# Performance work log

Measured on AMD Instinct MI355X. Metric: run time of the kernel, lower is better.

The kernel has to match this reference:

```python
import jax, jax.numpy as jnp
import numpy as np
import math

H = 64   # hidden_size
N = 512  # num_objects
B = 128  # batch


def setup_inputs() -> dict:
    key = jax.random.key(0)
    ks = jax.random.split(key, 10)
    q = jax.random.normal(ks[0], (N, B, H), dtype=jnp.float32)
    k = jax.random.normal(ks[1], (N, B, H), dtype=jnp.float32)
    v = jax.random.normal(ks[2], (N, B, H), dtype=jnp.float32)
    # binary visibility mask [B, N, N]
    batch_traffic_id_map = (jax.random.uniform(ks[3], (B, N, N)) < 0.7).astype(jnp.float32)
    s = 1.0 / math.sqrt(H)
    Wq = jax.random.uniform(ks[4], (H, H), minval=-s, maxval=s, dtype=jnp.float32)
    bq = jax.random.uniform(ks[5], (H,), minval=-s, maxval=s, dtype=jnp.float32)
    Wk = jax.random.uniform(ks[6], (H, H), minval=-s, maxval=s, dtype=jnp.float32)
    bk = jax.random.uniform(ks[7], (H,), minval=-s, maxval=s, dtype=jnp.float32)
    Wv = jax.random.uniform(ks[8], (H, H), minval=-s, maxval=s, dtype=jnp.float32)
    bv = jax.random.uniform(ks[9], (H,), minval=-s, maxval=s, dtype=jnp.float32)
    return {"q": q, "k": k, "v": v, "batch_traffic_id_map": batch_traffic_id_map,
            "Wq": Wq, "bq": bq, "Wk": Wk, "bk": bk, "Wv": Wv, "bv": bv}


def reference(q, k, v, batch_traffic_id_map, Wq, bq, Wk, bk, Wv, bv):
    hidden_size = q.shape[-1]
    # Linear projections then transpose(0,1): [N,B,H] -> [B,N,H]
    qp = jnp.einsum('nbh,kh->bnk', q, Wq) + bq
    kp = jnp.einsum('nbh,kh->bnk', k, Wk) + bk
    vp = jnp.einsum('nbh,kh->bnk', v, Wv) + bv
    # scaled scores, exp, mask, custom sum-normalization
    a = jnp.einsum('bnh,bmh->bnm', qp, kp) / jnp.sqrt(jnp.float32(hidden_size))
    a = jnp.exp(a) * batch_traffic_id_map
    a_sum = jnp.sum(a, axis=-1)                      # [B, N]
    a_sum = jnp.where(a_sum == 0, jnp.ones_like(a_sum), a_sum)
    A = a / a_sum[..., None]                          # [B, N, N]
    out = jnp.einsum('bnm,bmh->nbh', A, vp)           # matmul + transpose(0,1)
    # dropout is identity in eval mode
    return out, A
```

## Files before the change

kernel.cpp:

```cpp
#include <hip/hip_runtime.h>

#define H 64
#define NOBJ 512
#define BATCH 128

typedef __attribute__((ext_vector_type(8))) short s16x8;
typedef __attribute__((ext_vector_type(4))) float f32x4;
typedef __attribute__((ext_vector_type(4))) unsigned short u16x4;
typedef __attribute__((ext_vector_type(8))) unsigned short u16x8;

__device__ __forceinline__ unsigned short f2bf(float f) {
    unsigned int u = __float_as_uint(f);
    u += 0x7FFFu + ((u >> 16) & 1u);
    return (unsigned short)(u >> 16);
}
__device__ __forceinline__ float bf2f(unsigned short h) {
    return __uint_as_float((unsigned int)h << 16);
}

#define MFMA16(a, b, c) __builtin_amdgcn_mfma_f32_16x16x32_bf16(a, b, c, 0, 0, 0)

__global__ __launch_bounds__(256) void mask_pack_kernel(
    const float* __restrict__ mask, unsigned int* __restrict__ bits)
{
    __shared__ unsigned char nib[256];
    const int tid = threadIdx.x;
    const size_t base = (size_t)blockIdx.x * 1024;
    const float4 f = *(const float4*)(mask + base + (size_t)tid * 4);
    nib[tid] = (unsigned char)((unsigned)(f.x != 0.0f)
             | ((unsigned)(f.y != 0.0f) << 1)
             | ((unsigned)(f.z != 0.0f) << 2)
             | ((unsigned)(f.w != 0.0f) << 3));
    __syncthreads();
    if (tid < 32) {
        unsigned int wv = 0;
        #pragma unroll
        for (int i = 0; i < 8; ++i)
            wv |= (unsigned int)nib[tid * 8 + i] << (4 * i);
        bits[base / 32 + tid] = wv;
    }
}

__global__ __launch_bounds__(256) void proj_kernel(
    const float* __restrict__ q, const float* __restrict__ k, const float* __restrict__ v,
    const float* __restrict__ Wq, const float* __restrict__ bq,
    const float* __restrict__ Wk, const float* __restrict__ bk,
    const float* __restrict__ Wv, const float* __restrict__ bv,
    unsigned short* __restrict__ qh, unsigned short* __restrict__ ql,
    unsigned short* __restrict__ kh, unsigned short* __restrict__ kl,
    unsigned short* __restrict__ vt)
{
    __shared__ unsigned short vtile[64][72];

    const int z = blockIdx.z;
    const float* x; const float* W; const float* bias;
    unsigned short* yh; unsigned short* yl;
    if (z == 0)      { x = q; W = Wq; bias = bq; yh = qh; yl = ql; }
    else if (z == 1) { x = k; W = Wk; bias = bk; yh = kh; yl = kl; }
    else             { x = v; W = Wv; bias = bv; yh = nullptr; yl = nullptr; }

    const int tid  = threadIdx.x;
    const int lane = tid & 63;
    const int wt   = tid >> 6;
    const int l15  = lane & 15;
    const int lg   = lane >> 4;
    const int n0   = blockIdx.x * 64;
    const int b    = blockIdx.y;

    s16x8 wfh[4][2], wfl[4][2];
    #pragma unroll
    for (int ht = 0; ht < 4; ++ht) {
        #pragma unroll
        for (int kc = 0; kc < 2; ++kc) {
            const float* p = W + (ht * 16 + l15) * H + kc * 32 + lg * 8;
            float4 f0 = *(const float4*)p;
            float4 f1 = *(const float4*)(p + 4);
            float f[8] = {f0.x, f0.y, f0.z, f0.w, f1.x, f1.y, f1.z, f1.w};
            s16x8 hi8, lo8;
            #pragma unroll
            for (int j = 0; j < 8; ++j) {
                const unsigned short hb = f2bf(f[j]);
                hi8[j] = (short)hb;
                lo8[j] = (short)f2bf(f[j] - bf2f(hb));
            }
            wfh[ht][kc] = hi8; wfl[ht][kc] = lo8;
        }
    }

    const int n = n0 + wt * 16 + l15;
    const float* xr = x + ((size_t)n * BATCH + b) * H;
    s16x8 xfh[2], xfl[2];
    #pragma unroll
    for (int kc = 0; kc < 2; ++kc) {
        const float* p = xr + kc * 32 + lg * 8;
        float4 f0 = *(const float4*)p;
        float4 f1 = *(const float4*)(p + 4);
        float f[8] = {f0.x, f0.y, f0.z, f0.w, f1.x, f1.y, f1.z, f1.w};
        s16x8 hi8, lo8;
        #pragma unroll
        for (int j = 0; j < 8; ++j) {
            const unsigned short hb = f2bf(f[j]);
            hi8[j] = (short)hb;
            lo8[j] = (short)f2bf(f[j] - bf2f(hb));
        }
        xfh[kc] = hi8; xfl[kc] = lo8;
    }

    if (z < 2) {
        #pragma unroll
        for (int ht = 0; ht < 4; ++ht) {
            const float4 b4 = *(const float4*)(bias + ht * 16 + lg * 4);
            f32x4 acc = {b4.x, b4.y, b4.z, b4.w};
            acc = MFMA16(wfh[ht][0], xfh[0], acc);
            acc = MFMA16(wfh[ht][1], xfh[1], acc);
            acc = MFMA16(wfh[ht][0], xfl[0], acc);
            acc = MFMA16(wfh[ht][1], xfl[1], acc);
            acc = MFMA16(wfl[ht][0], xfh[0], acc);
            acc = MFMA16(wfl[ht][1], xfh[1], acc);
            u16x4 hv, lv;
            #pragma unroll
            for (int r = 0; r < 4; ++r) {
                const unsigned short hb = f2bf(acc[r]);
                hv[r] = hb;
                lv[r] = f2bf(acc[r] - bf2f(hb));
            }
            const size_t o = ((size_t)b * NOBJ + n) * H + ht * 16 + lg * 4;
            *(u16x4*)(yh + o) = hv;
            *(u16x4*)(yl + o) = lv;
        }
    } else {
        #pragma unroll
        for (int ht = 0; ht < 4; ++ht) {
            const float bs = bias[ht * 16 + l15];
            f32x4 acc = {bs, bs, bs, bs};
            acc = MFMA16(xfh[0], wfh[ht][0], acc);
            acc = MFMA16(xfh[1], wfh[ht][1], acc);
            acc = MFMA16(xfl[0], wfh[ht][0], acc);
            acc = MFMA16(xfl[1], wfh[ht][1], acc);
            acc = MFMA16(xfh[0], wfl[ht][0], acc);
            acc = MFMA16(xfh[1], wfl[ht][1], acc);
            u16x4 hv;
            #pragma unroll
            for (int r = 0; r < 4; ++r) hv[r] = f2bf(acc[r]);
            *(u16x4*)&vtile[ht * 16 + l15][wt * 16 + lg * 4] = hv;
        }
        __syncthreads();
        const int h = tid >> 2, nc = (tid & 3) * 16;
        const u16x8 d0 = *(const u16x8*)&vtile[h][nc];
        const u16x8 d1 = *(const u16x8*)&vtile[h][nc + 8];
        unsigned short* dst = vt + ((size_t)b * H + h) * NOBJ + n0 + nc;
        *(u16x8*)dst = d0;
        *(u16x8*)(dst + 8) = d1;
    }
}

__global__ __launch_bounds__(256, 4) void attn_kernel(
    const unsigned short* __restrict__ qh, const unsigned short* __restrict__ ql,
    const unsigned short* __restrict__ kh, const unsigned short* __restrict__ kl,
    const unsigned short* __restrict__ vt, const unsigned int* __restrict__ bits,
    float* __restrict__ out, float* __restrict__ Aout)
{
    __shared__ unsigned short sch[16][520];
    __shared__ unsigned short scl[16][520];
    __shared__ float rsum[4][16];
    __shared__ float inv[16];

    const int tid  = threadIdx.x;
    const int lane = tid & 63;
    const int w    = tid >> 6;
    const int l15  = lane & 15;
    const int lg   = lane >> 4;
    const int n0   = blockIdx.x * 16;
    const int b    = blockIdx.y;

    const size_t qoff = ((size_t)b * NOBJ + n0 + l15) * H + lg * 8;
    const s16x8 qfh0 = *(const s16x8*)(qh + qoff);
    const s16x8 qfh1 = *(const s16x8*)(qh + qoff + 32);
    const s16x8 qfl0 = *(const s16x8*)(ql + qoff);
    const s16x8 qfl1 = *(const s16x8*)(ql + qoff + 32);

    const unsigned short* khp = kh + ((size_t)b * NOBJ + w * 128 + l15) * H + lg * 8;
    const unsigned short* klp = kl + ((size_t)b * NOBJ + w * 128 + l15) * H + lg * 8;

    const uint4 mw = *(const uint4*)(bits + ((size_t)b * NOBJ + n0 + l15) * (NOBJ / 32) + w * 4);
    const unsigned mwa[4] = {mw.x, mw.y, mw.z, mw.w};

    f32x4 ev[8];
    float rp = 0.0f;

    s16x8 ka[2][4];
    ka[0][0] = *(const s16x8*)(khp);
    ka[0][1] = *(const s16x8*)(khp + 32);
    ka[0][2] = *(const s16x8*)(klp);
    ka[0][3] = *(const s16x8*)(klp + 32);

    #pragma unroll
    for (int mt = 0; mt < 8; ++mt) {
        const int cur = mt & 1, nxt = cur ^ 1;
        if (mt < 7) {
            const int o = (mt + 1) * 16 * H;
            ka[nxt][0] = *(const s16x8*)(khp + o);
            ka[nxt][1] = *(const s16x8*)(khp + o + 32);
            ka[nxt][2] = *(const s16x8*)(klp + o);
            ka[nxt][3] = *(const s16x8*)(klp + o + 32);
        }

        f32x4 acc = {0.0f, 0.0f, 0.0f, 0.0f};
        acc = MFMA16(ka[cur][0], qfh0, acc);
        acc = MFMA16(ka[cur][1], qfh1, acc);
        acc = MFMA16(ka[cur][0], qfl0, acc);
        acc = MFMA16(ka[cur][1], qfl1, acc);
        acc = MFMA16(ka[cur][2], qfh0, acc);
        acc = MFMA16(ka[cur][3], qfh1, acc);

        const unsigned wsel = mwa[mt >> 1] >> (((mt & 1) << 4) + (lg << 2));
        f32x4 e;
        #pragma unroll
        for (int r = 0; r < 4; ++r) {
            const float ex = __expf(acc[r] * 0.125f);
            e[r] = ((wsel >> r) & 1u) ? ex : 0.0f;
        }
        ev[mt] = e;
        rp += (e[0] + e[1]) + (e[2] + e[3]);

        u16x4 hv, lv;
        #pragma unroll
        for (int r = 0; r < 4; ++r) {
            const unsigned short hb = f2bf(e[r]);
            hv[r] = hb;
            lv[r] = f2bf(e[r] - bf2f(hb));
        }
        const int mo = w * 128 + mt * 16 + lg * 4;
        *(u16x4*)&sch[l15][mo] = hv;
        *(u16x4*)&scl[l15][mo] = lv;
    }

    rp += __shfl_xor(rp, 16);
    rp += __shfl_xor(rp, 32);
    if (lane < 16) rsum[w][lane] = rp;
    __syncthreads();
    if (tid < 16) {
        const float s = (rsum[0][tid] + rsum[1][tid]) + (rsum[2][tid] + rsum[3][tid]);
        inv[tid] = 1.0f / (s == 0.0f ? 1.0f : s);
    }
    __syncthreads();

    {
        const float iv = inv[l15];
        float* Arow = Aout + ((size_t)b * NOBJ + n0 + l15) * NOBJ + w * 128 + lg * 4;
        #pragma unroll
        for (int mt = 0; mt < 8; ++mt) {
            float4 a4;
            a4.x = ev[mt][0] * iv; a4.y = ev[mt][1] * iv;
            a4.z = ev[mt][2] * iv; a4.w = ev[mt][3] * iv;
            *(float4*)(Arow + mt * 16) = a4;
        }
    }

    const unsigned short* vtp = vt + ((size_t)b * H + w * 16 + l15) * NOBJ + lg * 8;
    f32x4 o0 = {0.0f, 0.0f, 0.0f, 0.0f}, o1 = {0.0f, 0.0f, 0.0f, 0.0f};
    #pragma unroll
    for (int ks = 0; ks < 16; ks += 2) {
        const int mk = ks * 32 + lg * 8;
        const s16x8 ah0 = *(const s16x8*)&sch[l15][mk];
        const s16x8 al0 = *(const s16x8*)&scl[l15][mk];
        const s16x8 vf0 = *(const s16x8*)(vtp + ks * 32);
        o0 = MFMA16(ah0, vf0, o0);
        o0 = MFMA16(al0, vf0, o0);
        const s16x8 ah1 = *(const s16x8*)&sch[l15][mk + 32];
        const s16x8 al1 = *(const s16x8*)&scl[l15][mk + 32];
        const s16x8 vf1 = *(const s16x8*)(vtp + ks * 32 + 32);
        o1 = MFMA16(ah1, vf1, o1);
        o1 = MFMA16(al1, vf1, o1);
    }

    #pragma unroll
    for (int r = 0; r < 4; ++r) {
        const int nn = lg * 4 + r;
        out[((size_t)(n0 + nn) * BATCH + b) * H + w * 16 + l15] = (o0[r] + o1[r]) * inv[nn];
    }
}

extern "C" void kernel_launch(void* const* d_in, const int* in_sizes, int n_in,
                              void* d_out, int out_size, void* d_ws, size_t ws_size,
                              hipStream_t stream)
{
    (void)in_sizes; (void)n_in; (void)out_size; (void)ws_size;
    const float* q    = (const float*)d_in[0];
    const float* k    = (const float*)d_in[1];
    const float* v    = (const float*)d_in[2];
    const float* mask = (const float*)d_in[3];
    const float* Wq   = (const float*)d_in[4];
    const float* bq   = (const float*)d_in[5];
    const float* Wk   = (const float*)d_in[6];
    const float* bk   = (const float*)d_in[7];
    const float* Wv   = (const float*)d_in[8];
    const float* bv   = (const float*)d_in[9];

    float* out  = (float*)d_out;
    float* Aout = (float*)d_out + (size_t)NOBJ * BATCH * H;

    const size_t S = (size_t)BATCH * NOBJ * H;
    unsigned short* qh = (unsigned short*)d_ws;
    unsigned short* ql = qh + S;
    unsigned short* kh = ql + S;
    unsigned short* kl = kh + S;
    unsigned short* vt = kl + S;
    unsigned int* bits = (unsigned int*)(vt + S);

    mask_pack_kernel<<<dim3((BATCH * NOBJ * NOBJ) / 1024), 256, 0, stream>>>(mask, bits);
    proj_kernel<<<dim3(NOBJ / 64, BATCH, 3), 256, 0, stream>>>(
        q, k, v, Wq, bq, Wk, bk, Wv, bv, qh, ql, kh, kl, vt);
    attn_kernel<<<dim3(NOBJ / 16, BATCH), 256, 0, stream>>>(
        qh, ql, kh, kl, vt, bits, out, Aout);
}
```

Before: 398.1 us.

## Merge mask-pack and projection kernels, remap attention grid per XCD, add nontemporal I/O

Mask packing and the projections now run as one kernel with a flat grid, where blockIdx selects either a pack block or a projection block. This saves one launch and lets both phases overlap. The attention grid is flattened and remapped so that consecutive blocks landing on the same XCD share a batch, for better L2 reuse of K and V. It also deepens K prefetch from two buffers to three and uses nontemporal loads for the mask and nontemporal stores for A and out. The extra K buffer raises register pressure under launch bounds of 4 waves.

```diff
diff --git a/kernel.cpp b/kernel.cpp
--- a/kernel.cpp
+++ b/kernel.cpp
@@ -3,6 +3,7 @@
 #define H 64
 #define NOBJ 512
 #define BATCH 128
+#define PACK_BLOCKS ((BATCH * NOBJ * NOBJ) / 1024)
 
 typedef __attribute__((ext_vector_type(8))) short s16x8;
 typedef __attribute__((ext_vector_type(4))) float f32x4;
@@ -20,28 +21,8 @@
 
 #define MFMA16(a, b, c) __builtin_amdgcn_mfma_f32_16x16x32_bf16(a, b, c, 0, 0, 0)
 
-__global__ __launch_bounds__(256) void mask_pack_kernel(
-    const float* __restrict__ mask, unsigned int* __restrict__ bits)
-{
-    __shared__ unsigned char nib[256];
-    const int tid = threadIdx.x;
-    const size_t base = (size_t)blockIdx.x * 1024;
-    const float4 f = *(const float4*)(mask + base + (size_t)tid * 4);
-    nib[tid] = (unsigned char)((unsigned)(f.x != 0.0f)
-             | ((unsigned)(f.y != 0.0f) << 1)
-             | ((unsigned)(f.z != 0.0f) << 2)
-             | ((unsigned)(f.w != 0.0f) << 3));
-    __syncthreads();
-    if (tid < 32) {
-        unsigned int wv = 0;
-        #pragma unroll
-        for (int i = 0; i < 8; ++i)
-            wv |= (unsigned int)nib[tid * 8 + i] << (4 * i);
-        bits[base / 32 + tid] = wv;
-    }
-}
-
-__global__ __launch_bounds__(256) void proj_kernel(
+__global__ __launch_bounds__(256) void prep_kernel(
+    const float* __restrict__ mask, unsigned int* __restrict__ bits,
     const float* __restrict__ q, const float* __restrict__ k, const float* __restrict__ v,
     const float* __restrict__ Wq, const float* __restrict__ bq,
     const float* __restrict__ Wk, const float* __restrict__ bk,
@@ -51,30 +32,52 @@
     unsigned short* __restrict__ vt)
 {
     __shared__ unsigned short vtile[64][72];
-
-    const int z = blockIdx.z;
+    const int tid = threadIdx.x;
+
+    if (blockIdx.x < PACK_BLOCKS) {
+        unsigned char* nib = (unsigned char*)&vtile[0][0];
+        const size_t base = (size_t)blockIdx.x * 1024;
+        const f32x4 f = __builtin_nontemporal_load((const f32x4*)(mask + base + (size_t)tid * 4));
+        nib[tid] = (unsigned char)((unsigned)(f[0] != 0.0f)
+                 | ((unsigned)(f[1] != 0.0f) << 1)
+                 | ((unsigned)(f[2] != 0.0f) << 2)
+                 | ((unsigned)(f[3] != 0.0f) << 3));
+        __syncthreads();
+        if (tid < 32) {
+            unsigned int wv = 0;
+            #pragma unroll
+            for (int i = 0; i < 8; ++i)
+                wv |= (unsigned int)nib[tid * 8 + i] << (4 * i);
+            bits[base / 32 + tid] = wv;
+        }
+        return;
+    }
+
+    const int p   = blockIdx.x - PACK_BLOCKS;
+    const int z   = p >> 10;
+    const int rem = p & 1023;
+    const int b   = rem >> 3;
+    const int n0  = (rem & 7) * 64;
+
     const float* x; const float* W; const float* bias;
     unsigned short* yh; unsigned short* yl;
     if (z == 0)      { x = q; W = Wq; bias = bq; yh = qh; yl = ql; }
     else if (z == 1) { x = k; W = Wk; bias = bk; yh = kh; yl = kl; }
     else             { x = v; W = Wv; bias = bv; yh = nullptr; yl = nullptr; }
 
-    const int tid  = threadIdx.x;
     const int lane = tid & 63;
     const int wt   = tid >> 6;
     const int l15  = lane & 15;
     const int lg   = lane >> 4;
-    const int n0   = blockIdx.x * 64;
-    const int b    = blockIdx.y;
 
     s16x8 wfh[4][2], wfl[4][2];
     #pragma unroll
     for (int ht = 0; ht < 4; ++ht) {
         #pragma unroll
         for (int kc = 0; kc < 2; ++kc) {
-            const float* p = W + (ht * 16 + l15) * H + kc * 32 + lg * 8;
-            float4 f0 = *(const float4*)p;
-            float4 f1 = *(const float4*)(p + 4);
+            const float* wp = W + (ht * 16 + l15) * H + kc * 32 + lg * 8;
+            float4 f0 = *(const float4*)wp;
+            float4 f1 = *(const float4*)(wp + 4);
             float f[8] = {f0.x, f0.y, f0.z, f0.w, f1.x, f1.y, f1.z, f1.w};
             s16x8 hi8, lo8;
             #pragma unroll
@@ -92,9 +95,9 @@
     s16x8 xfh[2], xfl[2];
     #pragma unroll
     for (int kc = 0; kc < 2; ++kc) {
-        const float* p = xr + kc * 32 + lg * 8;
-        float4 f0 = *(const float4*)p;
-        float4 f1 = *(const float4*)(p + 4);
+        const float* xp = xr + kc * 32 + lg * 8;
+        float4 f0 = *(const float4*)xp;
+        float4 f1 = *(const float4*)(xp + 4);
         float f[8] = {f0.x, f0.y, f0.z, f0.w, f1.x, f1.y, f1.z, f1.w};
         s16x8 hi8, lo8;
         #pragma unroll
@@ -170,8 +173,12 @@
     const int w    = tid >> 6;
     const int l15  = lane & 15;
     const int lg   = lane >> 4;
-    const int n0   = blockIdx.x * 16;
-    const int b    = blockIdx.y;
+
+    const int orig = blockIdx.x;
+    const int xcd  = orig & 7;
+    const int s    = orig >> 3;
+    const int b    = xcd + 8 * (s >> 5);
+    const int n0   = (s & 31) * 16;
 
     const size_t qoff = ((size_t)b * NOBJ + n0 + l15) * H + lg * 8;
     const s16x8 qfh0 = *(const s16x8*)(qh + qoff);
@@ -188,22 +195,23 @@
     f32x4 ev[8];
     float rp = 0.0f;
 
-    s16x8 ka[2][4];
-    ka[0][0] = *(const s16x8*)(khp);
-    ka[0][1] = *(const s16x8*)(khp + 32);
-    ka[0][2] = *(const s16x8*)(klp);
-    ka[0][3] = *(const s16x8*)(klp + 32);
+    s16x8 ka[3][4];
+#define LOADK(buf, mi)                                              \
+    do {                                                            \
+        const int _o = (mi) * 16 * H;                               \
+        ka[buf][0] = *(const s16x8*)(khp + _o);                     \
+        ka[buf][1] = *(const s16x8*)(khp + _o + 32);                \
+        ka[buf][2] = *(const s16x8*)(klp + _o);                     \
+        ka[buf][3] = *(const s16x8*)(klp + _o + 32);                \
+    } while (0)
+
+    LOADK(0, 0);
+    LOADK(1, 1);
 
     #pragma unroll
     for (int mt = 0; mt < 8; ++mt) {
-        const int cur = mt & 1, nxt = cur ^ 1;
-        if (mt < 7) {
-            const int o = (mt + 1) * 16 * H;
-            ka[nxt][0] = *(const s16x8*)(khp + o);
-            ka[nxt][1] = *(const s16x8*)(khp + o + 32);
-            ka[nxt][2] = *(const s16x8*)(klp + o);
-            ka[nxt][3] = *(const s16x8*)(klp + o + 32);
-        }
+        const int cur = mt % 3;
+        if (mt < 6) LOADK((mt + 2) % 3, mt + 2);
 
         f32x4 acc = {0.0f, 0.0f, 0.0f, 0.0f};
         acc = MFMA16(ka[cur][0], qfh0, acc);
@@ -234,14 +242,15 @@
         *(u16x4*)&sch[l15][mo] = hv;
         *(u16x4*)&scl[l15][mo] = lv;
     }
+#undef LOADK
 
     rp += __shfl_xor(rp, 16);
     rp += __shfl_xor(rp, 32);
     if (lane < 16) rsum[w][lane] = rp;
     __syncthreads();
     if (tid < 16) {
-        const float s = (rsum[0][tid] + rsum[1][tid]) + (rsum[2][tid] + rsum[3][tid]);
-        inv[tid] = 1.0f / (s == 0.0f ? 1.0f : s);
+        const float sv = (rsum[0][tid] + rsum[1][tid]) + (rsum[2][tid] + rsum[3][tid]);
+        inv[tid] = 1.0f / (sv == 0.0f ? 1.0f : sv);
     }
     __syncthreads();
 
@@ -250,10 +259,10 @@
         float* Arow = Aout + ((size_t)b * NOBJ + n0 + l15) * NOBJ + w * 128 + lg * 4;
         #pragma unroll
         for (int mt = 0; mt < 8; ++mt) {
-            float4 a4;
-            a4.x = ev[mt][0] * iv; a4.y = ev[mt][1] * iv;
-            a4.z = ev[mt][2] * iv; a4.w = ev[mt][3] * iv;
-            *(float4*)(Arow + mt * 16) = a4;
+            f32x4 a4;
+            a4[0] = ev[mt][0] * iv; a4[1] = ev[mt][1] * iv;
+            a4[2] = ev[mt][2] * iv; a4[3] = ev[mt][3] * iv;
+            __builtin_nontemporal_store(a4, (f32x4*)(Arow + mt * 16));
         }
     }
 
@@ -277,7 +286,8 @@
     #pragma unroll
     for (int r = 0; r < 4; ++r) {
         const int nn = lg * 4 + r;
-        out[((size_t)(n0 + nn) * BATCH + b) * H + w * 16 + l15] = (o0[r] + o1[r]) * inv[nn];
+        __builtin_nontemporal_store((o0[r] + o1[r]) * inv[nn],
+            out + ((size_t)(n0 + nn) * BATCH + b) * H + w * 16 + l15);
     }
 }
 
@@ -308,9 +318,8 @@
     unsigned short* vt = kl + S;
     unsigned int* bits = (unsigned int*)(vt + S);
 
-    mask_pack_kernel<<<dim3((BATCH * NOBJ * NOBJ) / 1024), 256, 0, stream>>>(mask, bits);
-    proj_kernel<<<dim3(NOBJ / 64, BATCH, 3), 256, 0, stream>>>(
-        q, k, v, Wq, bq, Wk, bk, Wv, bv, qh, ql, kh, kl, vt);
-    attn_kernel<<<dim3(NOBJ / 16, BATCH), 256, 0, stream>>>(
+    prep_kernel<<<dim3(PACK_BLOCKS + 3 * BATCH * (NOBJ / 64)), 256, 0, stream>>>(
+        mask, bits, q, k, v, Wq, bq, Wk, bk, Wv, bv, qh, ql, kh, kl, vt);
+    attn_kernel<<<dim3((NOBJ / 16) * BATCH), 256, 0, stream>>>(
         qh, ql, kh, kl, vt, bits, out, Aout);
 }
```

After: 406.7 us. 1.02x slower.
